# Optimization experiments

Measured on AMD Instinct MI355X. Metric: run time of the kernel, lower is better.

Reference implementation:

```python
import jax, jax.numpy as jnp
import numpy as np

T, N, D = 8, 100000, 128
E, MS = 50000, 4
H0, H1 = 64, 32
EPS = 1e-8  # torch.cosine_similarity eps


def setup_inputs() -> dict:
    key = jax.random.key(0)
    ks = jax.random.split(key, 12)
    edge_list = jax.random.randint(ks[0], (E, 2), 0, N, dtype=jnp.int64)
    z1 = jax.random.normal(ks[1], (T, N, D), dtype=jnp.float32)
    z2 = jax.random.normal(ks[2], (T, N, D), dtype=jnp.float32)
    w1 = jax.random.normal(ks[3], (MS, D), dtype=jnp.float32)
    w2 = jax.random.normal(ks[4], (MS, D), dtype=jnp.float32)
    # MLP: Linear(T, H0) -> ReLU -> Linear(H0, H1) -> ReLU -> Linear(H1, 1)
    W0 = jax.random.normal(ks[5], (H0, T), dtype=jnp.float32) * (1.0 / np.sqrt(T))
    b0 = jnp.zeros((H0,), dtype=jnp.float32)
    W1 = jax.random.normal(ks[6], (H1, H0), dtype=jnp.float32) * (1.0 / np.sqrt(H0))
    b1 = jnp.zeros((H1,), dtype=jnp.float32)
    Wp = jax.random.normal(ks[7], (1, H1), dtype=jnp.float32) * (1.0 / np.sqrt(H1))
    bp = jnp.zeros((1,), dtype=jnp.float32)
    return {"edge_list": edge_list, "z1_trains": z1, "z2_trains": z2,
            "weight_vec1": w1, "weight_vec2": w2,
            "W0": W0, "b0": b0, "W1": W1, "b1": b1, "Wp": Wp, "bp": bp}


def _head_avg_weighted_cos(z, w, src, dst):
    # z: [T,N,D], w: [MS,D] -> mean over heads of cos(w*a, w*b): [T,E]
    a = z[:, src, :]            # [T,E,D] gather
    b = z[:, dst, :]            # [T,E,D] gather
    wsq = w * w                 # [MS,D]
    dot = jnp.einsum('ted,md->tem', a * b, wsq)
    na = jnp.sqrt(jnp.einsum('ted,md->tem', a * a, wsq))
    nb = jnp.sqrt(jnp.einsum('ted,md->tem', b * b, wsq))
    cos = dot / (jnp.maximum(na, EPS) * jnp.maximum(nb, EPS))
    return jnp.mean(cos, axis=-1)  # average over MS heads -> [T,E]


def reference(edge_list, z1_trains, z2_trains, weight_vec1, weight_vec2,
              W0, b0, W1, b1, Wp, bp):
    src = edge_list[:, 0]
    dst = edge_list[:, 1]
    # Only sim_emb_1 feeds the MLP in the original forward (sim_emb_2/sim unused).
    s1 = _head_avg_weighted_cos(z1_trains, weight_vec1, src, dst)  # [T,E]
    sim_emb_1 = s1.T                                               # [E,T]
    h = jax.nn.relu(sim_emb_1 @ W0.T + b0)   # dropout p used at eval -> identity
    h = jax.nn.relu(h @ W1.T + b1)
    pred = h @ Wp.T + bp                     # [E,1]
    return pred.reshape(-1)
```

## Files before the change

### kernel.cpp

```cpp
#include <hip/hip_runtime.h>
#include <math.h>

#define T_DIM   8
#define N_NODES 100000
#define D_DIM   128
#define E_EDGES 50000
#define H0_DIM  64
#define H1_DIM  32
#define EPS_F   1e-8f

__global__ __launch_bounds__(256) void fused_edge_cos_mlp(
    const int*   __restrict__ edge_list,
    const float* __restrict__ z1,
    const float* __restrict__ w1,
    const float* __restrict__ W0,
    const float* __restrict__ b0,
    const float* __restrict__ W1,
    const float* __restrict__ b1,
    const float* __restrict__ Wp,
    const float* __restrict__ bp,
    float*       __restrict__ out)
{
    __shared__ float lds_h0[4 * 64];

    const int tid  = threadIdx.x;
    const int wave = tid >> 6;
    const int l    = tid & 63;
    const int e    = blockIdx.x * 4 + wave;

    const int g  = l >> 4;
    const int m  = (l >> 2) & 3;
    const int q  = l & 3;
    const int d0 = q * 32;

    const int src = edge_list[2 * e];
    const int dst = edge_list[2 * e + 1];

    float4 wsq[8];
    {
        const float4* wp4 = reinterpret_cast<const float4*>(w1 + m * D_DIM + d0);
        #pragma unroll
        for (int j = 0; j < 8; ++j) {
            float4 w = wp4[j];
            wsq[j] = make_float4(w.x * w.x, w.y * w.y, w.z * w.z, w.w * w.w);
        }
    }

    float pab[2], paa[2], pbb[2];
    #pragma unroll
    for (int r = 0; r < 2; ++r) {
        const int t = g + 4 * r;
        const float4* arow = reinterpret_cast<const float4*>(
            z1 + ((size_t)t * N_NODES + src) * D_DIM + d0);
        const float4* brow = reinterpret_cast<const float4*>(
            z1 + ((size_t)t * N_NODES + dst) * D_DIM + d0);

        float s_ab = 0.f, s_aa = 0.f, s_bb = 0.f;
        #pragma unroll
        for (int j = 0; j < 8; ++j) {
            float4 a = arow[j];
            float4 b = brow[j];
            float4 w = wsq[j];
            s_ab = fmaf(a.x * b.x, w.x, s_ab);
            s_ab = fmaf(a.y * b.y, w.y, s_ab);
            s_ab = fmaf(a.z * b.z, w.z, s_ab);
            s_ab = fmaf(a.w * b.w, w.w, s_ab);
            s_aa = fmaf(a.x * a.x, w.x, s_aa);
            s_aa = fmaf(a.y * a.y, w.y, s_aa);
            s_aa = fmaf(a.z * a.z, w.z, s_aa);
            s_aa = fmaf(a.w * a.w, w.w, s_aa);
            s_bb = fmaf(b.x * b.x, w.x, s_bb);
            s_bb = fmaf(b.y * b.y, w.y, s_bb);
            s_bb = fmaf(b.z * b.z, w.z, s_bb);
            s_bb = fmaf(b.w * b.w, w.w, s_bb);
        }
        pab[r] = s_ab; paa[r] = s_aa; pbb[r] = s_bb;
    }

    #pragma unroll
    for (int r = 0; r < 2; ++r) {
        pab[r] += __shfl_xor(pab[r], 1); pab[r] += __shfl_xor(pab[r], 2);
        paa[r] += __shfl_xor(paa[r], 1); paa[r] += __shfl_xor(paa[r], 2);
        pbb[r] += __shfl_xor(pbb[r], 1); pbb[r] += __shfl_xor(pbb[r], 2);
    }

    float simr[2];
    #pragma unroll
    for (int r = 0; r < 2; ++r) {
        float na = sqrtf(paa[r]);
        float nb = sqrtf(pbb[r]);
        float c  = pab[r] / (fmaxf(na, EPS_F) * fmaxf(nb, EPS_F));
        c += __shfl_xor(c, 4);
        c += __shfl_xor(c, 8);
        simr[r] = 0.25f * c;
    }

    float st[8];
    #pragma unroll
    for (int t = 0; t < 4; ++t) {
        st[t]     = __shfl(simr[0], t * 16);
        st[t + 4] = __shfl(simr[1], t * 16);
    }

    {
        const float4* w0p = reinterpret_cast<const float4*>(W0 + l * T_DIM);
        float4 wa = w0p[0];
        float4 wb = w0p[1];
        float acc = b0[l];
        acc = fmaf(st[0], wa.x, acc); acc = fmaf(st[1], wa.y, acc);
        acc = fmaf(st[2], wa.z, acc); acc = fmaf(st[3], wa.w, acc);
        acc = fmaf(st[4], wb.x, acc); acc = fmaf(st[5], wb.y, acc);
        acc = fmaf(st[6], wb.z, acc); acc = fmaf(st[7], wb.w, acc);
        lds_h0[wave * 64 + l] = fmaxf(acc, 0.f);
    }
    __syncthreads();

    {
        const int k = l & 31;
        const float4* w1p = reinterpret_cast<const float4*>(W1 + k * H0_DIM);
        const float4* h0p = reinterpret_cast<const float4*>(&lds_h0[wave * 64]);
        float acc = b1[k];
        #pragma unroll
        for (int jj = 0; jj < 16; ++jj) {
            float4 wv = w1p[jj];
            float4 hv = h0p[jj];
            acc = fmaf(wv.x, hv.x, acc);
            acc = fmaf(wv.y, hv.y, acc);
            acc = fmaf(wv.z, hv.z, acc);
            acc = fmaf(wv.w, hv.w, acc);
        }
        float p = fmaxf(acc, 0.f) * Wp[k];
        p += __shfl_xor(p, 1);
        p += __shfl_xor(p, 2);
        p += __shfl_xor(p, 4);
        p += __shfl_xor(p, 8);
        p += __shfl_xor(p, 16);
        if (l == 0) out[e] = p + bp[0];
    }
}

extern "C" void kernel_launch(void* const* d_in, const int* in_sizes, int n_in,
                              void* d_out, int out_size, void* d_ws, size_t ws_size,
                              hipStream_t stream) {
    const int*   edge_list = (const int*)  d_in[0];
    const float* z1        = (const float*)d_in[1];
    const float* w1        = (const float*)d_in[3];
    const float* W0        = (const float*)d_in[5];
    const float* b0        = (const float*)d_in[6];
    const float* W1        = (const float*)d_in[7];
    const float* b1        = (const float*)d_in[8];
    const float* Wp        = (const float*)d_in[9];
    const float* bp        = (const float*)d_in[10];
    float*       out       = (float*)d_out;

    dim3 block(256);
    dim3 grid(E_EDGES / 4);
    fused_edge_cos_mlp<<<grid, block, 0, stream>>>(
        edge_list, z1, w1, W0, b0, W1, b1, Wp, bp, out);
}
```

Baseline: 882.2 us.

## Remap lanes to load each z row once and stage squared head weights in LDS

Before, each element of the source and destination rows was loaded four times, once per head, because lanes were split across heads. Lanes now map to (timestep, 16-wide chunk) pairs, so each wave reads each row exactly once into registers and loops over the four heads locally. The squared head weights are computed once per block and kept in shared memory. The change cuts redundant global gather traffic, at the cost of an extra block barrier and more FMA work and registers per lane.

```diff
diff --git a/kernel.cpp b/kernel.cpp
--- a/kernel.cpp
+++ b/kernel.cpp
@@ -21,86 +21,92 @@
     const float* __restrict__ bp,
     float*       __restrict__ out)
 {
-    __shared__ float lds_h0[4 * 64];
+    __shared__ float wsq_lds[4 * D_DIM];
+    __shared__ float lds_h0[4 * H0_DIM];
 
     const int tid  = threadIdx.x;
     const int wave = tid >> 6;
     const int l    = tid & 63;
     const int e    = blockIdx.x * 4 + wave;
 
-    const int g  = l >> 4;
-    const int m  = (l >> 2) & 3;
-    const int q  = l & 3;
-    const int d0 = q * 32;
+    {
+        const float2* w2p = reinterpret_cast<const float2*>(w1);
+        float2 w = w2p[tid];
+        wsq_lds[2 * tid]     = w.x * w.x;
+        wsq_lds[2 * tid + 1] = w.y * w.y;
+    }
+
+    const int t  = l >> 3;
+    const int c  = l & 7;
+    const int d0 = c * 16;
 
     const int src = edge_list[2 * e];
     const int dst = edge_list[2 * e + 1];
 
-    float4 wsq[8];
-    {
-        const float4* wp4 = reinterpret_cast<const float4*>(w1 + m * D_DIM + d0);
+    const float4* arow = reinterpret_cast<const float4*>(
+        z1 + ((size_t)t * N_NODES + src) * D_DIM + d0);
+    const float4* brow = reinterpret_cast<const float4*>(
+        z1 + ((size_t)t * N_NODES + dst) * D_DIM + d0);
+    float4 av[4], bv[4];
+    #pragma unroll
+    for (int j = 0; j < 4; ++j) av[j] = arow[j];
+    #pragma unroll
+    for (int j = 0; j < 4; ++j) bv[j] = brow[j];
+
+    __syncthreads();
+
+    float s_ab[4], s_aa[4], s_bb[4];
+    #pragma unroll
+    for (int m = 0; m < 4; ++m) { s_ab[m] = 0.f; s_aa[m] = 0.f; s_bb[m] = 0.f; }
+
+    #pragma unroll
+    for (int m = 0; m < 4; ++m) {
+        const float4* wq = reinterpret_cast<const float4*>(&wsq_lds[m * D_DIM + d0]);
         #pragma unroll
-        for (int j = 0; j < 8; ++j) {
-            float4 w = wp4[j];
-            wsq[j] = make_float4(w.x * w.x, w.y * w.y, w.z * w.z, w.w * w.w);
+        for (int j = 0; j < 4; ++j) {
+            float4 a = av[j];
+            float4 b = bv[j];
+            float4 w = wq[j];
+            s_ab[m] = fmaf(a.x * b.x, w.x, s_ab[m]);
+            s_ab[m] = fmaf(a.y * b.y, w.y, s_ab[m]);
+            s_ab[m] = fmaf(a.z * b.z, w.z, s_ab[m]);
+            s_ab[m] = fmaf(a.w * b.w, w.w, s_ab[m]);
+            s_aa[m] = fmaf(a.x * a.x, w.x, s_aa[m]);
+            s_aa[m] = fmaf(a.y * a.y, w.y, s_aa[m]);
+            s_aa[m] = fmaf(a.z * a.z, w.z, s_aa[m]);
+            s_aa[m] = fmaf(a.w * a.w, w.w, s_aa[m]);
+            s_bb[m] = fmaf(b.x * b.x, w.x, s_bb[m]);
+            s_bb[m] = fmaf(b.y * b.y, w.y, s_bb[m]);
+            s_bb[m] = fmaf(b.z * b.z, w.z, s_bb[m]);
+            s_bb[m] = fmaf(b.w * b.w, w.w, s_bb[m]);
         }
     }
 
-    float pab[2], paa[2], pbb[2];
     #pragma unroll
-    for (int r = 0; r < 2; ++r) {
-        const int t = g + 4 * r;
-        const float4* arow = reinterpret_cast<const float4*>(
-            z1 + ((size_t)t * N_NODES + src) * D_DIM + d0);
-        const float4* brow = reinterpret_cast<const float4*>(
-            z1 + ((size_t)t * N_NODES + dst) * D_DIM + d0);
-
-        float s_ab = 0.f, s_aa = 0.f, s_bb = 0.f;
-        #pragma unroll
-        for (int j = 0; j < 8; ++j) {
-            float4 a = arow[j];
-            float4 b = brow[j];
-            float4 w = wsq[j];
-            s_ab = fmaf(a.x * b.x, w.x, s_ab);
-            s_ab = fmaf(a.y * b.y, w.y, s_ab);
-            s_ab = fmaf(a.z * b.z, w.z, s_ab);
-            s_ab = fmaf(a.w * b.w, w.w, s_ab);
-            s_aa = fmaf(a.x * a.x, w.x, s_aa);
-            s_aa = fmaf(a.y * a.y, w.y, s_aa);
-            s_aa = fmaf(a.z * a.z, w.z, s_aa);
-            s_aa = fmaf(a.w * a.w, w.w, s_aa);
-            s_bb = fmaf(b.x * b.x, w.x, s_bb);
-            s_bb = fmaf(b.y * b.y, w.y, s_bb);
-            s_bb = fmaf(b.z * b.z, w.z, s_bb);
-            s_bb = fmaf(b.w * b.w, w.w, s_bb);
-        }
-        pab[r] = s_ab; paa[r] = s_aa; pbb[r] = s_bb;
+    for (int m = 0; m < 4; ++m) {
+        s_ab[m] += __shfl_xor(s_ab[m], 1);
+        s_ab[m] += __shfl_xor(s_ab[m], 2);
+        s_ab[m] += __shfl_xor(s_ab[m], 4);
+        s_aa[m] += __shfl_xor(s_aa[m], 1);
+        s_aa[m] += __shfl_xor(s_aa[m], 2);
+        s_aa[m] += __shfl_xor(s_aa[m], 4);
+        s_bb[m] += __shfl_xor(s_bb[m], 1);
+        s_bb[m] += __shfl_xor(s_bb[m], 2);
+        s_bb[m] += __shfl_xor(s_bb[m], 4);
     }
 
+    float sim = 0.f;
     #pragma unroll
-    for (int r = 0; r < 2; ++r) {
-        pab[r] += __shfl_xor(pab[r], 1); pab[r] += __shfl_xor(pab[r], 2);
-        paa[r] += __shfl_xor(paa[r], 1); paa[r] += __shfl_xor(paa[r], 2);
-        pbb[r] += __shfl_xor(pbb[r], 1); pbb[r] += __shfl_xor(pbb[r], 2);
+    for (int m = 0; m < 4; ++m) {
+        float na = sqrtf(s_aa[m]);
+        float nb = sqrtf(s_bb[m]);
+        sim += s_ab[m] / (fmaxf(na, EPS_F) * fmaxf(nb, EPS_F));
     }
-
-    float simr[2];
-    #pragma unroll
-    for (int r = 0; r < 2; ++r) {
-        float na = sqrtf(paa[r]);
-        float nb = sqrtf(pbb[r]);
-        float c  = pab[r] / (fmaxf(na, EPS_F) * fmaxf(nb, EPS_F));
-        c += __shfl_xor(c, 4);
-        c += __shfl_xor(c, 8);
-        simr[r] = 0.25f * c;
-    }
+    sim *= 0.25f;
 
     float st[8];
     #pragma unroll
-    for (int t = 0; t < 4; ++t) {
-        st[t]     = __shfl(simr[0], t * 16);
-        st[t + 4] = __shfl(simr[1], t * 16);
-    }
+    for (int tt = 0; tt < 8; ++tt) st[tt] = __shfl(sim, tt * 8);
 
     {
         const float4* w0p = reinterpret_cast<const float4*>(W0 + l * T_DIM);
@@ -111,14 +117,14 @@
         acc = fmaf(st[2], wa.z, acc); acc = fmaf(st[3], wa.w, acc);
         acc = fmaf(st[4], wb.x, acc); acc = fmaf(st[5], wb.y, acc);
         acc = fmaf(st[6], wb.z, acc); acc = fmaf(st[7], wb.w, acc);
-        lds_h0[wave * 64 + l] = fmaxf(acc, 0.f);
+        lds_h0[wave * H0_DIM + l] = fmaxf(acc, 0.f);
     }
     __syncthreads();
 
     {
         const int k = l & 31;
         const float4* w1p = reinterpret_cast<const float4*>(W1 + k * H0_DIM);
-        const float4* h0p = reinterpret_cast<const float4*>(&lds_h0[wave * 64]);
+        const float4* h0p = reinterpret_cast<const float4*>(&lds_h0[wave * H0_DIM]);
         float acc = b1[k];
         #pragma unroll
         for (int jj = 0; jj < 16; ++jj) {
```

After: 729.5 us. 17.3% less time.
